# Kernel tuning notes

Hardware: AMD Instinct MI355X
Metric: run time of the kernel (lower is better)

Reference implementation:

```python
import jax, jax.numpy as jnp
import numpy as np

RANK = 200
N_ENT = 200_000
N_REL = 500
NNZ = 500_000


def setup_inputs() -> dict:
    key = jax.random.key(0)
    k1, k2, k3, k4, k5 = jax.random.split(key, 5)
    # xavier_normal_ init: std = sqrt(2 / (fan_in + fan_out))
    a = jax.random.normal(k1, (N_ENT, RANK), dtype=jnp.float32) * np.float32(np.sqrt(2.0 / (N_ENT + RANK)))
    b = jax.random.normal(k2, (N_REL, RANK), dtype=jnp.float32) * np.float32(np.sqrt(2.0 / (N_REL + RANK)))
    subj = jax.random.randint(k3, (NNZ,), 0, N_ENT)
    rel = jax.random.randint(k4, (NNZ,), 0, N_REL)
    obj = jax.random.randint(k5, (NNZ,), 0, N_ENT)
    coo_ns = jnp.stack([subj, rel, obj], axis=1)  # [nnz, 3]
    vals_ns = jnp.ones((NNZ,), dtype=jnp.float32)  # observed tensor values (positives)
    return {"coo_ns": coo_ns, "vals_ns": vals_ns, "a": a, "b": b}


def reference(coo_ns, vals_ns, a, b):
    # Gather factor rows for each nonzero coordinate (irregular gather)
    a0 = a[coo_ns[:, 0], :]  # [nnz, R] subject entity rows
    b1 = b[coo_ns[:, 1], :]  # [nnz, R] relation rows
    a2 = a[coo_ns[:, 2], :]  # [nnz, R] object entity rows

    # Khatri-Rao style elementwise product + rank reduction
    kruskal_val = jnp.sum(a0 * b1 * a2, axis=1)  # [nnz]

    # squared-error GCP loss and its derivative w.r.t. kruskal_val
    diff = kruskal_val - vals_ns
    loss = diff * diff                 # [nnz]
    deriv = 2.0 * diff                 # [nnz]

    # per-nonzero MTTKRP gradient rows (mttcrp1 with same-coordinate trick)
    g_a = deriv[:, None] * b1 * a2     # mode 0
    g_b = deriv[:, None] * a0 * a2     # mode 1
    g_c = deriv[:, None] * a0 * b1     # mode 2

    # scatter (overwrite, as in a_torch.grad[a_elems,:] = g_a etc.)
    grad_a = jnp.zeros_like(a).at[coo_ns[:, 0]].set(g_a).at[coo_ns[:, 2]].set(g_c)
    grad_b = jnp.zeros_like(b).at[coo_ns[:, 1]].set(g_b)
    return loss, grad_a, grad_b
```

## Files before the change

### kernel.cpp

```cpp
#include <hip/hip_runtime.h>
#include <hip/hip_bf16.h>

#define RANK   200
#define N_ENT  200000
#define N_REL  500
#define NNZ    500000
#define NB_WIN 256
#define WB_PAD 512

typedef float f32x4 __attribute__((ext_vector_type(4)));

__device__ __forceinline__ void nt_store4(float* p,
                                          float a, float b_, float c, float d) {
    f32x4 v = {a, b_, c, d};
    __builtin_nontemporal_store(v, (f32x4*)p);
}

__global__ void winner_kernel(const int* __restrict__ coo,
                              int* __restrict__ wA,
                              int* __restrict__ partial_wB) {
    __shared__ int lwB[WB_PAD];
    for (int t = threadIdx.x; t < WB_PAD; t += blockDim.x) lwB[t] = -1;
    __syncthreads();

    int gtid   = blockIdx.x * blockDim.x + threadIdx.x;
    int stride = gridDim.x * blockDim.x;
    for (int i = gtid; i < NNZ; i += stride) {
        int s = coo[3 * i + 0];
        int r = coo[3 * i + 1];
        int o = coo[3 * i + 2];
        atomicMax(&wA[s], i);
        atomicMax(&wA[o], NNZ + i);
        atomicMax(&lwB[r], i);
    }
    __syncthreads();
    int* out = partial_wB + (size_t)blockIdx.x * WB_PAD;
    for (int t = threadIdx.x; t < WB_PAD; t += blockDim.x) out[t] = lwB[t];
}

__global__ void wb_reduce_kernel(const int* __restrict__ partial_wB,
                                 int* __restrict__ wB) {
    int t = threadIdx.x;
    int m = -1;
    for (int nb = 0; nb < NB_WIN; ++nb)
        m = max(m, partial_wB[(size_t)nb * WB_PAD + t]);
    if (t < N_REL) wB[t] = m;
}

__global__ void fused_kernel(const int* __restrict__ coo,
                             const float* __restrict__ vals,
                             const float* __restrict__ a,
                             const float* __restrict__ b,
                             const int* __restrict__ wA,
                             const int* __restrict__ wB,
                             float* __restrict__ loss,
                             float* __restrict__ grad_a,
                             float* __restrict__ grad_b) {
    int wave = (blockIdx.x * blockDim.x + threadIdx.x) >> 6;
    int lane = threadIdx.x & 63;
    if (wave >= NNZ) return;
    int s = coo[3 * wave + 0];
    int r = coo[3 * wave + 1];
    int o = coo[3 * wave + 2];
    int ks = wA[s];
    int ko = wA[o];
    int kr = wB[r];

    float4 x = make_float4(0.f, 0.f, 0.f, 0.f);
    float4 y = x, z = x;
    float sum = 0.0f;
    if (lane < RANK / 4) {
        x = ((const float4*)(a + (size_t)s * RANK))[lane];
        y = ((const float4*)(b + (size_t)r * RANK))[lane];
        z = ((const float4*)(a + (size_t)o * RANK))[lane];
        sum = x.x * y.x * z.x + x.y * y.y * z.y
            + x.z * y.z * z.z + x.w * y.w * z.w;
    }
    #pragma unroll
    for (int off = 32; off > 0; off >>= 1)
        sum += __shfl_xor(sum, off, 64);

    float d = sum - vals[wave];
    if (lane == 0) __builtin_nontemporal_store(d * d, &loss[wave]);
    float d2 = 2.0f * d;

    if (lane < RANK / 4) {
        if (ks == wave) {
            float* outp = grad_a + (size_t)s * RANK + lane * 4;
            nt_store4(outp, d2 * y.x * z.x, d2 * y.y * z.y,
                            d2 * y.z * z.z, d2 * y.w * z.w);
        }
        if (ko == NNZ + wave) {
            float* outp = grad_a + (size_t)o * RANK + lane * 4;
            nt_store4(outp, d2 * x.x * y.x, d2 * x.y * y.y,
                            d2 * x.z * y.z, d2 * x.w * y.w);
        }
        if (kr == wave) {
            float* outp = grad_b + (size_t)r * RANK + lane * 4;
            nt_store4(outp, d2 * x.x * z.x, d2 * x.y * z.y,
                            d2 * x.z * z.z, d2 * x.w * z.w);
        }
    }
}

__global__ void zero_untouched_kernel(const int* __restrict__ wA,
                                      const int* __restrict__ wB,
                                      float* __restrict__ grad_a,
                                      float* __restrict__ grad_b) {
    int tid  = blockIdx.x * blockDim.x + threadIdx.x;
    int lane = threadIdx.x & 63;
    bool need = false;
    if (tid < N_ENT) {
        need = (wA[tid] < 0);
    } else if (tid < N_ENT + N_REL) {
        need = (wB[tid - N_ENT] < 0);
    }
    unsigned long long mask = __ballot(need);
    while (mask) {
        int src = __ffsll((long long)mask) - 1;
        mask &= mask - 1;
        int rowsel = __shfl(tid, src, 64);
        float* outp = (rowsel < N_ENT)
            ? (grad_a + (size_t)rowsel * RANK)
            : (grad_b + (size_t)(rowsel - N_ENT) * RANK);
        if (lane < RANK / 4)
            nt_store4(outp + lane * 4, 0.f, 0.f, 0.f, 0.f);
    }
}

extern "C" void kernel_launch(void* const* d_in, const int* in_sizes, int n_in,
                              void* d_out, int out_size, void* d_ws, size_t ws_size,
                              hipStream_t stream) {
    const int*   coo  = (const int*)d_in[0];
    const float* vals = (const float*)d_in[1];
    const float* a    = (const float*)d_in[2];
    const float* b    = (const float*)d_in[3];

    float* loss   = (float*)d_out;
    float* grad_a = loss + NNZ;
    float* grad_b = grad_a + (size_t)N_ENT * RANK;

    int* wA         = (int*)d_ws;
    int* wB         = wA + N_ENT;
    int* partial_wB = wB + WB_PAD;

    (void)hipMemsetAsync(wA, 0xFF, (size_t)N_ENT * sizeof(int), stream);

    winner_kernel<<<NB_WIN, 256, 0, stream>>>(coo, wA, partial_wB);
    wb_reduce_kernel<<<1, WB_PAD, 0, stream>>>(partial_wB, wB);
    {
        long long total = (long long)NNZ * 64;
        int threads = 256;
        long long blocks = (total + threads - 1) / threads;
        fused_kernel<<<(int)blocks, threads, 0, stream>>>(coo, vals, a, b, wA, wB,
                                                          loss, grad_a, grad_b);
    }
    {
        int total   = N_ENT + N_REL;
        int threads = 256;
        int blocks  = (total + threads - 1) / threads;
        zero_untouched_kernel<<<blocks, threads, 0, stream>>>(wA, wB, grad_a, grad_b);
    }
}
```

Measured before the change: 439.5 us.

## Merge all phases into one cooperative persistent kernel with grid syncs

Replaces the memset plus four separate launches (winner election, relation-winner reduce, fused loss/gradient, zeroing of untouched rows) with one cooperative kernel of 1024 blocks. The phases are separated by grid.sync, and the main phase walks the nonzeros with a grid-stride loop over waves. This removes launch and inter-kernel gaps and folds the wA reset into the kernel. In exchange it caps resident waves for the latency-bound gather phase and adds grid-wide barrier costs. If the cooperative launch fails, the old multi-kernel path runs instead.

```diff
diff --git a/kernel.cpp b/kernel.cpp
--- a/kernel.cpp
+++ b/kernel.cpp
@@ -1,12 +1,16 @@
 #include <hip/hip_runtime.h>
 #include <hip/hip_bf16.h>
-
-#define RANK   200
-#define N_ENT  200000
-#define N_REL  500
-#define NNZ    500000
-#define NB_WIN 256
-#define WB_PAD 512
+#include <hip/hip_cooperative_groups.h>
+
+namespace cg = cooperative_groups;
+
+#define RANK    200
+#define N_ENT   200000
+#define N_REL   500
+#define NNZ     500000
+#define NB_WIN  256
+#define NB_COOP 1024
+#define WB_PAD  512
 
 typedef float f32x4 __attribute__((ext_vector_type(4)));
 
@@ -14,6 +18,117 @@
                                           float a, float b_, float c, float d) {
     f32x4 v = {a, b_, c, d};
     __builtin_nontemporal_store(v, (f32x4*)p);
+}
+
+
+__global__ void __launch_bounds__(256, 4) mega_kernel(
+        const int* __restrict__ coo, const float* __restrict__ vals,
+        const float* __restrict__ a, const float* __restrict__ b,
+        float* __restrict__ loss, float* __restrict__ grad_a,
+        float* __restrict__ grad_b, int* __restrict__ wA,
+        int* __restrict__ wB, int* __restrict__ partial_wB) {
+    cg::grid_group grid = cg::this_grid();
+    __shared__ int lwB[WB_PAD];
+    const int tid  = threadIdx.x;
+    const int gtid = blockIdx.x * blockDim.x + tid;
+    const int gsz  = gridDim.x * blockDim.x;
+    const int lane = tid & 63;
+
+    for (int t = tid; t < WB_PAD; t += blockDim.x) lwB[t] = -1;
+    for (int t = gtid; t < N_ENT; t += gsz) wA[t] = -1;
+    __syncthreads();
+    __threadfence();
+    grid.sync();
+
+    for (int i = gtid; i < NNZ; i += gsz) {
+        int s = coo[3 * i + 0];
+        int r = coo[3 * i + 1];
+        int o = coo[3 * i + 2];
+        atomicMax(&wA[s], i);
+        atomicMax(&wA[o], NNZ + i);
+        atomicMax(&lwB[r], i);
+    }
+    __syncthreads();
+    for (int t = tid; t < WB_PAD; t += blockDim.x)
+        partial_wB[(size_t)blockIdx.x * WB_PAD + t] = lwB[t];
+    __threadfence();
+    grid.sync();
+
+    int wid = gtid >> 6;
+    if (wid < WB_PAD) {
+        int m = -1;
+        for (int k = lane; k < NB_COOP; k += 64)
+            m = max(m, partial_wB[(size_t)k * WB_PAD + wid]);
+        #pragma unroll
+        for (int off = 32; off > 0; off >>= 1)
+            m = max(m, __shfl_xor(m, off, 64));
+        if (lane == 0) wB[wid] = m;
+    }
+    __threadfence();
+    grid.sync();
+
+    const int nwaves = gsz >> 6;
+    for (int i = (gtid >> 6); i < NNZ; i += nwaves) {
+        int s = coo[3 * i + 0];
+        int r = coo[3 * i + 1];
+        int o = coo[3 * i + 2];
+        int ks = wA[s];
+        int ko = wA[o];
+        int kr = wB[r];
+
+        float4 x = make_float4(0.f, 0.f, 0.f, 0.f);
+        float4 y = x, z = x;
+        float sum = 0.0f;
+        if (lane < RANK / 4) {
+            x = ((const float4*)(a + (size_t)s * RANK))[lane];
+            y = ((const float4*)(b + (size_t)r * RANK))[lane];
+            z = ((const float4*)(a + (size_t)o * RANK))[lane];
+            sum = x.x * y.x * z.x + x.y * y.y * z.y
+                + x.z * y.z * z.z + x.w * y.w * z.w;
+        }
+        #pragma unroll
+        for (int off = 32; off > 0; off >>= 1)
+            sum += __shfl_xor(sum, off, 64);
+
+        float d = sum - vals[i];
+        if (lane == 0) __builtin_nontemporal_store(d * d, &loss[i]);
+        float d2 = 2.0f * d;
+
+        if (lane < RANK / 4) {
+            if (ks == i) {
+                float* outp = grad_a + (size_t)s * RANK + lane * 4;
+                nt_store4(outp, d2 * y.x * z.x, d2 * y.y * z.y,
+                                d2 * y.z * z.z, d2 * y.w * z.w);
+            }
+            if (ko == NNZ + i) {
+                float* outp = grad_a + (size_t)o * RANK + lane * 4;
+                nt_store4(outp, d2 * x.x * y.x, d2 * x.y * y.y,
+                                d2 * x.z * y.z, d2 * x.w * y.w);
+            }
+            if (kr == i) {
+                float* outp = grad_b + (size_t)r * RANK + lane * 4;
+                nt_store4(outp, d2 * x.x * z.x, d2 * x.y * z.y,
+                                d2 * x.z * z.z, d2 * x.w * z.w);
+            }
+        }
+    }
+
+    {
+        bool need = false;
+        if (gtid < N_ENT)                   need = (wA[gtid] < 0);
+        else if (gtid < N_ENT + N_REL)      need = (wB[gtid - N_ENT] < 0);
+        unsigned long long mask = __ballot(need);
+        while (mask) {
+            int src = __ffsll((long long)mask) - 1;
+            mask &= mask - 1;
+            int rowsel = __shfl(gtid, src, 64);
+            float* outp = (rowsel < N_ENT)
+                ? (grad_a + (size_t)rowsel * RANK)
+                : (grad_b + (size_t)(rowsel - N_ENT) * RANK);
+            if (lane < RANK / 4)
+                nt_store4(outp + lane * 4, 0.f, 0.f, 0.f, 0.f);
+        }
+    }
 }
 
 __global__ void winner_kernel(const int* __restrict__ coo,
@@ -144,21 +259,29 @@
     int* wB         = wA + N_ENT;
     int* partial_wB = wB + WB_PAD;
 
-    (void)hipMemsetAsync(wA, 0xFF, (size_t)N_ENT * sizeof(int), stream);
-
-    winner_kernel<<<NB_WIN, 256, 0, stream>>>(coo, wA, partial_wB);
-    wb_reduce_kernel<<<1, WB_PAD, 0, stream>>>(partial_wB, wB);
-    {
-        long long total = (long long)NNZ * 64;
-        int threads = 256;
-        long long blocks = (total + threads - 1) / threads;
-        fused_kernel<<<(int)blocks, threads, 0, stream>>>(coo, vals, a, b, wA, wB,
-                                                          loss, grad_a, grad_b);
-    }
-    {
-        int total   = N_ENT + N_REL;
-        int threads = 256;
-        int blocks  = (total + threads - 1) / threads;
-        zero_untouched_kernel<<<blocks, threads, 0, stream>>>(wA, wB, grad_a, grad_b);
-    }
-}
+    void* args[] = {(void*)&coo, (void*)&vals, (void*)&a, (void*)&b,
+                    (void*)&loss, (void*)&grad_a, (void*)&grad_b,
+                    (void*)&wA, (void*)&wB, (void*)&partial_wB};
+    hipError_t err = hipLaunchCooperativeKernel(
+        (const void*)mega_kernel, dim3(NB_COOP), dim3(256), args, 0, stream);
+
+    if (err != hipSuccess) {
+        (void)hipMemsetAsync(wA, 0xFF, (size_t)N_ENT * sizeof(int), stream);
+        winner_kernel<<<NB_WIN, 256, 0, stream>>>(coo, wA, partial_wB);
+        wb_reduce_kernel<<<1, WB_PAD, 0, stream>>>(partial_wB, wB);
+        {
+            long long total = (long long)NNZ * 64;
+            int threads = 256;
+            long long blocks = (total + threads - 1) / threads;
+            fused_kernel<<<(int)blocks, threads, 0, stream>>>(
+                coo, vals, a, b, wA, wB, loss, grad_a, grad_b);
+        }
+        {
+            int total   = N_ENT + N_REL;
+            int threads = 256;
+            int blocks  = (total + threads - 1) / threads;
+            zero_untouched_kernel<<<blocks, threads, 0, stream>>>(
+                wA, wB, grad_a, grad_b);
+        }
+    }
+}
```

Result: slower. 943.9 us (+114.8%).

## Fuse zeroing into main kernel and replace wB reduction with spread global atomics

Applied to the files above, without the earlier changes.

Removes the separate wB reduction kernel by doing relation-winner atomics directly in global memory, with entries spread 16 ints apart to reduce same-line contention. The winner kernel now uses one thread per nonzero instead of a grid-stride loop. Zeroing of untouched gradient rows is folded into the tail of the fused kernel, indexed by wave id, which saves a launch. In exchange, each wave does an extra check, and global atomics on only 500 hot relation slots may contend.

```diff
diff --git a/kernel.cpp b/kernel.cpp
--- a/kernel.cpp
+++ b/kernel.cpp
@@ -5,8 +5,7 @@
 #define N_ENT  200000
 #define N_REL  500
 #define NNZ    500000
-#define NB_WIN 256
-#define WB_PAD 512
+#define WB_STRIDE 16
 
 typedef float f32x4 __attribute__((ext_vector_type(4)));
 
@@ -18,33 +17,15 @@
 
 __global__ void winner_kernel(const int* __restrict__ coo,
                               int* __restrict__ wA,
-                              int* __restrict__ partial_wB) {
-    __shared__ int lwB[WB_PAD];
-    for (int t = threadIdx.x; t < WB_PAD; t += blockDim.x) lwB[t] = -1;
-    __syncthreads();
-
-    int gtid   = blockIdx.x * blockDim.x + threadIdx.x;
-    int stride = gridDim.x * blockDim.x;
-    for (int i = gtid; i < NNZ; i += stride) {
-        int s = coo[3 * i + 0];
-        int r = coo[3 * i + 1];
-        int o = coo[3 * i + 2];
-        atomicMax(&wA[s], i);
-        atomicMax(&wA[o], NNZ + i);
-        atomicMax(&lwB[r], i);
-    }
-    __syncthreads();
-    int* out = partial_wB + (size_t)blockIdx.x * WB_PAD;
-    for (int t = threadIdx.x; t < WB_PAD; t += blockDim.x) out[t] = lwB[t];
-}
-
-__global__ void wb_reduce_kernel(const int* __restrict__ partial_wB,
-                                 int* __restrict__ wB) {
-    int t = threadIdx.x;
-    int m = -1;
-    for (int nb = 0; nb < NB_WIN; ++nb)
-        m = max(m, partial_wB[(size_t)nb * WB_PAD + t]);
-    if (t < N_REL) wB[t] = m;
+                              int* __restrict__ wB_spread) {
+    int i = blockIdx.x * blockDim.x + threadIdx.x;
+    if (i >= NNZ) return;
+    int s = coo[3 * i + 0];
+    int r = coo[3 * i + 1];
+    int o = coo[3 * i + 2];
+    atomicMax(&wA[s], i);
+    atomicMax(&wA[o], NNZ + i);
+    atomicMax(&wB_spread[r * WB_STRIDE], i);
 }
 
 __global__ void fused_kernel(const int* __restrict__ coo,
@@ -52,7 +33,7 @@
                              const float* __restrict__ a,
                              const float* __restrict__ b,
                              const int* __restrict__ wA,
-                             const int* __restrict__ wB,
+                             const int* __restrict__ wB_spread,
                              float* __restrict__ loss,
                              float* __restrict__ grad_a,
                              float* __restrict__ grad_b) {
@@ -64,7 +45,7 @@
     int o = coo[3 * wave + 2];
     int ks = wA[s];
     int ko = wA[o];
-    int kr = wB[r];
+    int kr = wB_spread[r * WB_STRIDE];
 
     float4 x = make_float4(0.f, 0.f, 0.f, 0.f);
     float4 y = x, z = x;
@@ -101,30 +82,17 @@
                             d2 * x.z * z.z, d2 * x.w * z.w);
         }
     }
-}
 
-__global__ void zero_untouched_kernel(const int* __restrict__ wA,
-                                      const int* __restrict__ wB,
-                                      float* __restrict__ grad_a,
-                                      float* __restrict__ grad_b) {
-    int tid  = blockIdx.x * blockDim.x + threadIdx.x;
-    int lane = threadIdx.x & 63;
-    bool need = false;
-    if (tid < N_ENT) {
-        need = (wA[tid] < 0);
-    } else if (tid < N_ENT + N_REL) {
-        need = (wB[tid - N_ENT] < 0);
-    }
-    unsigned long long mask = __ballot(need);
-    while (mask) {
-        int src = __ffsll((long long)mask) - 1;
-        mask &= mask - 1;
-        int rowsel = __shfl(tid, src, 64);
-        float* outp = (rowsel < N_ENT)
-            ? (grad_a + (size_t)rowsel * RANK)
-            : (grad_b + (size_t)(rowsel - N_ENT) * RANK);
-        if (lane < RANK / 4)
-            nt_store4(outp + lane * 4, 0.f, 0.f, 0.f, 0.f);
+    if (wave < N_ENT + N_REL) {
+        bool is_ent = wave < N_ENT;
+        int key = is_ent ? wA[wave] : wB_spread[(wave - N_ENT) * WB_STRIDE];
+        if (key < 0) {
+            float* outp = is_ent
+                ? (grad_a + (size_t)wave * RANK)
+                : (grad_b + (size_t)(wave - N_ENT) * RANK);
+            if (lane < RANK / 4)
+                nt_store4(outp + lane * 4, 0.f, 0.f, 0.f, 0.f);
+        }
     }
 }
 
@@ -140,25 +108,24 @@
     float* grad_a = loss + NNZ;
     float* grad_b = grad_a + (size_t)N_ENT * RANK;
 
-    int* wA         = (int*)d_ws;
-    int* wB         = wA + N_ENT;
-    int* partial_wB = wB + WB_PAD;
+    int* wA        = (int*)d_ws;
+    int* wB_spread = wA + N_ENT;
 
-    (void)hipMemsetAsync(wA, 0xFF, (size_t)N_ENT * sizeof(int), stream);
+    (void)hipMemsetAsync(wA, 0xFF,
+                         (size_t)(N_ENT + N_REL * WB_STRIDE) * sizeof(int),
+                         stream);
 
-    winner_kernel<<<NB_WIN, 256, 0, stream>>>(coo, wA, partial_wB);
-    wb_reduce_kernel<<<1, WB_PAD, 0, stream>>>(partial_wB, wB);
+    {
+        int threads = 256;
+        int blocks  = (NNZ + threads - 1) / threads;
+        winner_kernel<<<blocks, threads, 0, stream>>>(coo, wA, wB_spread);
+    }
     {
         long long total = (long long)NNZ * 64;
         int threads = 256;
         long long blocks = (total + threads - 1) / threads;
-        fused_kernel<<<(int)blocks, threads, 0, stream>>>(coo, vals, a, b, wA, wB,
+        fused_kernel<<<(int)blocks, threads, 0, stream>>>(coo, vals, a, b,
+                                                          wA, wB_spread,
                                                           loss, grad_a, grad_b);
     }
-    {
-        int total   = N_ENT + N_REL;
-        int threads = 256;
-        int blocks  = (total + threads - 1) / threads;
-        zero_untouched_kernel<<<blocks, threads, 0, stream>>>(wA, wB, grad_a, grad_b);
-    }
 }
```

New measurement: 450.3 us. 2.5% more time.
